# Kernel tuning notes

Hardware: AMD Instinct MI355X
Metric: run time of the kernel (lower is better)

The kernel has to match this reference:

```python
import jax, jax.numpy as jnp
import numpy as np

L = 2          # num_blocks
E = 256        # embed_features
FIN = 64       # input_features
FF = 4 * E     # dim_feedforward
OUT = 10       # out_dim
WCTX = 64      # context_len
B, S = 2, 1024
LN_EPS = 1e-5


def _ln(x, g, b):
    m = jnp.mean(x, axis=-1, keepdims=True)
    v = jnp.mean((x - m) ** 2, axis=-1, keepdims=True)
    return (x - m) / jnp.sqrt(v + LN_EPS) * g + b


def setup_inputs() -> dict:
    key = jax.random.key(0)
    ks = jax.random.split(key, 12)
    s = 0.02
    return {
        "inputs": jax.random.normal(ks[0], (B, S, FIN), jnp.float32),
        "embed_w": jax.random.normal(ks[1], (E, FIN), jnp.float32) * s,
        "embed_b": jnp.zeros((E,), jnp.float32),
        "qkv_w": jax.random.normal(ks[2], (L, 3 * E, E), jnp.float32) * s,
        "qkv_b": jnp.zeros((L, 3 * E), jnp.float32),
        "attn_out_w": jax.random.normal(ks[3], (L, E, E), jnp.float32) * s,
        "attn_out_b": jnp.zeros((L, E), jnp.float32),
        "ln1_g": jnp.ones((L, E), jnp.float32),
        "ln1_b": jnp.zeros((L, E), jnp.float32),
        "ffn1_w": jax.random.normal(ks[4], (L, FF, E), jnp.float32) * s,
        "ffn1_b": jnp.zeros((L, FF), jnp.float32),
        "ffn2_w": jax.random.normal(ks[5], (L, E, FF), jnp.float32) * s,
        "ffn2_b": jnp.zeros((L, E), jnp.float32),
        "ln2_g": jnp.ones((L, E), jnp.float32),
        "ln2_b": jnp.zeros((L, E), jnp.float32),
        "head_w": jax.random.normal(ks[6], (OUT, E), jnp.float32) * s,
        "head_b": jnp.zeros((OUT,), jnp.float32),
        "context_len": WCTX,
    }


def reference(inputs, embed_w, embed_b, qkv_w, qkv_b, attn_out_w, attn_out_b,
              ln1_g, ln1_b, ffn1_w, ffn1_b, ffn2_w, ffn2_b, ln2_g, ln2_b,
              head_w, head_b, context_len):
    b, s, _ = inputs.shape
    e = embed_w.shape[0]
    nh = max(1, e // 64) * 2           # torch: nhead = max(1, E//64)*2
    hd = e // nh
    scale = 1.0 / np.sqrt(hd)
    w = context_len

    emb = inputs @ embed_w.T + embed_b                       # [B,S,E]
    # left-pad with W-1 zeros so window pos p = padded[p:p+W] (zeros for early pos)
    padded = jnp.pad(emb, ((0, 0), (w - 1, 0), (0, 0)))
    idx = jnp.arange(s)[:, None] + jnp.arange(w)[None, :]    # [S,W]
    x = padded[:, idx].reshape(b * s, w, e)                  # [B*S,W,E]

    nlayers = qkv_w.shape[0]
    for l in range(nlayers):
        qkv = x @ qkv_w[l].T + qkv_b[l]                      # [N,W,3E]
        q, k, v = jnp.split(qkv, 3, axis=-1)
        q = q.reshape(-1, w, nh, hd)
        k = k.reshape(-1, w, nh, hd)
        v = v.reshape(-1, w, nh, hd)
        scores = jnp.einsum('nqhd,nkhd->nhqk', q, k) * scale
        attn = jax.nn.softmax(scores, axis=-1)
        o = jnp.einsum('nhqk,nkhd->nqhd', attn, v).reshape(-1, w, e)
        o = o @ attn_out_w[l].T + attn_out_b[l]
        x = _ln(x + o, ln1_g[l], ln1_b[l])                   # post-norm (torch default)
        ff = jax.nn.silu(x @ ffn1_w[l].T + ffn1_b[l]) @ ffn2_w[l].T + ffn2_b[l]
        x = _ln(x + ff, ln2_g[l], ln2_b[l])

    out = x[:, -1, :] @ head_w.T + head_b                    # last token of each window
    return out.reshape(b, s, -1)
```

## Files before the change

kernel.cpp:

```cpp
#include <hip/hip_runtime.h>
#include <hip/hip_bf16.h>

#define BB_ 2
#define SS_ 1024
#define FIN_ 64
#define EE_ 256
#define FF_ 1024
#define NH_ 8
#define HD_ 32
#define OUT_ 10
#define NWIN (BB_ * SS_)
#define NT 512
#define SCALE_ 0.17677669529663687f
#define XBP 264
#define TPAD 1088

typedef unsigned short u16;
typedef unsigned int u32;
typedef __attribute__((ext_vector_type(8))) short bf8_t;
typedef __attribute__((ext_vector_type(4))) float f4_t;
#define MFMA_B16(a, b, c) __builtin_amdgcn_mfma_f32_16x16x32_bf16(a, b, c, 0, 0, 0)

__device__ __forceinline__ u16 bf16r(float f) {
    u32 u = __builtin_bit_cast(u32, f);
    return (u16)((u + 0x7FFFu + ((u >> 16) & 1u)) >> 16);
}
__device__ __forceinline__ u32 pk_bf16(float a, float b) {
    return (u32)bf16r(a) | ((u32)bf16r(b) << 16);
}
__device__ __forceinline__ float b2f(u16 h) {
    return __builtin_bit_cast(float, ((u32)h) << 16);
}
__device__ __forceinline__ float b2f_lo(u32 u) {
    return __builtin_bit_cast(float, u << 16);
}
__device__ __forceinline__ float b2f_hi(u32 u) {
    return __builtin_bit_cast(float, u & 0xFFFF0000u);
}

__device__ __forceinline__ float dot4(float4 a, float4 b) {
    return a.x * b.x + a.y * b.y + a.z * b.z + a.w * b.w;
}
__device__ __forceinline__ float wsum(float v) {
#pragma unroll
    for (int o = 32; o > 0; o >>= 1) v += __shfl_xor(v, o, 64);
    return v;
}
__device__ __forceinline__ float wmax(float v) {
#pragma unroll
    for (int o = 32; o > 0; o >>= 1) v = fmaxf(v, __shfl_xor(v, o, 64));
    return v;
}
__device__ __forceinline__ float silu_f(float h) { return h / (1.f + __expf(-h)); }

struct CvtArgs {
    const float* s[9];
    u16* d[9];
    int n[9];
};

__global__ void k_pre(const float* __restrict__ in, const float* __restrict__ embw,
                      const float* __restrict__ embb, const float* __restrict__ qkv_b,
                      CvtArgs ca, float* __restrict__ emb, u16* __restrict__ qkvp) {
    __shared__ float row[FIN_];
    const int blk = blockIdx.x;
    const int tid = threadIdx.x;
    if (blk < 2048) {
        if (tid < FIN_) row[tid] = in[blk * FIN_ + tid];
        __syncthreads();
        const float4* w4 = (const float4*)(embw + tid * FIN_);
        const float4* r4 = (const float4*)row;
        float s = 0.f;
#pragma unroll
        for (int c = 0; c < FIN_ / 4; ++c) s += dot4(w4[c], r4[c]);
        emb[blk * EE_ + tid] = s + embb[tid];
    } else if (blk < 2816) {
        const int b2 = blk - 2048;
#pragma unroll 1
        for (int seg = 0; seg < 9; ++seg) {
            const float* __restrict__ src = ca.s[seg];
            u16* __restrict__ dst = ca.d[seg];
            const int nn = ca.n[seg];
            for (int i = b2 * 256 + tid; i < nn; i += 768 * 256)
                dst[i] = bf16r(src[i]);
        }
    } else {
        const int b3 = blk - 2816;
        for (int f = b3 * 256 + tid; f < 2 * 64 * 768; f += 8 * 256) {
            const int bat = f / 49152;
            const int rem = f - bat * 49152;
            const int r = rem / 768, cl = rem - r * 768;
            qkvp[((size_t)bat * TPAD + r) * 768 + cl] = bf16r(qkv_b[cl]);
        }
    }
}

__global__ __launch_bounds__(512) void k_qkv0m(const float* __restrict__ emb,
                                               const u16* __restrict__ wq0b,
                                               const float* __restrict__ qkvb,
                                               u16* __restrict__ qkvp) {
    __shared__ u16 ab[16 * XBP];
    const int b = blockIdx.x;
    const int tid = threadIdx.x, lane = tid & 63, wv = tid >> 6;
    const int col = lane & 15, quad = lane >> 4;
    for (int idx = tid; idx < 16 * 256; idx += 512) {
        const int i = idx >> 8, e = idx & 255;
        ab[i * XBP + e] = bf16r(emb[(b * 16 + i) * EE_ + e]);
    }
    __syncthreads();
    f4_t acc[6];
#pragma unroll
    for (int nt = 0; nt < 6; ++nt) acc[nt] = (f4_t){0.f, 0.f, 0.f, 0.f};
#pragma unroll
    for (int ks = 0; ks < 8; ++ks) {
        const bf8_t ax = *(const bf8_t*)(ab + col * XBP + ks * 32 + quad * 8);
#pragma unroll
        for (int nt = 0; nt < 6; ++nt) {
            const int r = wv * 96 + nt * 16 + col;
            const bf8_t bw = *(const bf8_t*)(wq0b + r * EE_ + ks * 32 + quad * 8);
            acc[nt] = MFMA_B16(ax, bw, acc[nt]);
        }
    }
#pragma unroll
    for (int nt = 0; nt < 6; ++nt) {
        const int cc = wv * 96 + nt * 16 + col;
        const float bs = qkvb[cc];
#pragma unroll
        for (int j = 0; j < 4; ++j) {
            const int tok = b * 16 + quad * 4 + j;
            const int bb = tok >> 10;
            const size_t ti = (size_t)bb * TPAD + (tok & 1023) + 64;
            qkvp[ti * 768 + cc] = bf16r(acc[nt][j] + bs);
        }
    }
}

__device__ __forceinline__ void reg_ln(float (&x)[2][4][4], float* red, float* stat,
                                       u16* xb,
                                       float gc0, float gc1, float bc0, float bc1,
                                       int tid, int wv, int col, int quad,
                                       int colg0, int colg1) {
    float ps[4][4], pq[4][4];
#pragma unroll
    for (int mt = 0; mt < 4; ++mt)
#pragma unroll
        for (int j = 0; j < 4; ++j) {
            const float v0 = x[0][mt][j], v1 = x[1][mt][j];
            ps[mt][j] = v0 + v1;
            pq[mt][j] = v0 * v0 + v1 * v1;
        }
#pragma unroll
    for (int o = 1; o < 16; o <<= 1) {
#pragma unroll
        for (int mt = 0; mt < 4; ++mt)
#pragma unroll
            for (int j = 0; j < 4; ++j) {
                ps[mt][j] += __shfl_xor(ps[mt][j], o);
                pq[mt][j] += __shfl_xor(pq[mt][j], o);
            }
    }
    if (col == 0) {
#pragma unroll
        for (int mt = 0; mt < 4; ++mt)
#pragma unroll
            for (int j = 0; j < 4; ++j) {
                const int row = mt * 16 + quad * 4 + j;
                red[row * 17 + wv * 2] = ps[mt][j];
                red[row * 17 + wv * 2 + 1] = pq[mt][j];
            }
    }
    __syncthreads();
    if (tid < 64) {
        float s = 0.f, q = 0.f;
#pragma unroll
        for (int w = 0; w < 8; ++w) {
            s += red[tid * 17 + w * 2];
            q += red[tid * 17 + w * 2 + 1];
        }
        const float m = s * 0.00390625f;
        const float var = q * 0.00390625f - m * m;
        stat[tid * 2] = m;
        stat[tid * 2 + 1] = rsqrtf(var + 1e-5f);
    }
    __syncthreads();
#pragma unroll
    for (int mt = 0; mt < 4; ++mt)
#pragma unroll
        for (int j = 0; j < 4; ++j) {
            const int row = mt * 16 + quad * 4 + j;
            const float m = stat[row * 2];
            const float rs = stat[row * 2 + 1];
            const float xn0 = (x[0][mt][j] - m) * rs * gc0 + bc0;
            const float xn1 = (x[1][mt][j] - m) * rs * gc1 + bc1;
            x[0][mt][j] = xn0;
            x[1][mt][j] = xn1;
            const u32 w = pk_bf16(xn0, xn1);
            xb[row * XBP + colg0] = (u16)w;
            xb[row * XBP + colg1] = (u16)(w >> 16);
        }
}

struct __align__(16) SMemA {
    union {
        struct { u16 qkpb[9216]; u16 vt[4608]; u16 pb[9216]; } att;
        struct { float red[64 * 17]; float stat[128]; } ln;
    } r1;
    u16 obxb[64 * XBP];
};

__global__ __launch_bounds__(NT, 4) void k_attn(
    const float* __restrict__ emb, const u16* __restrict__ qkvp,
    const u16* __restrict__ wob, const float* __restrict__ aob,
    const float* __restrict__ ln1g, const float* __restrict__ ln1b,
    u16* __restrict__ xbg) {
    __shared__ SMemA sm;
    const int n = blockIdx.x;
    const int bb = n >> 10, p = n & 1023;
    const int tid = threadIdx.x;
    const int lane = tid & 63, wv = tid >> 6;
    const int col = lane & 15, quad = lane >> 4;
    const int colg0 = wv * 32 + col, colg1 = colg0 + 16;

    for (int hp = 0; hp < 4; ++hp) {
        {
            const int i = tid >> 3, dg = tid & 7;
            const size_t rb = ((size_t)bb * TPAD + (p + 1 + i)) * 768 + hp * 64 + dg * 8;
            const uint4 q4 = *(const uint4*)(qkvp + rb);
            const uint4 k4 = *(const uint4*)(qkvp + rb + 256);
            const uint4 v4 = *(const uint4*)(qkvp + rb + 512);
            *(uint4*)(sm.r1.att.qkpb + i * 72 + dg * 8) = q4;
            *(uint4*)(sm.r1.att.qkpb + 4608 + i * 72 + dg * 8) = k4;
            union { uint4 u; u16 h[8]; } vu; vu.u = v4;
#pragma unroll
            for (int c = 0; c < 8; ++c)
                sm.r1.att.vt[(dg * 8 + c) * 72 + i] = vu.h[c];
        }
        __syncthreads();
        const int hh = wv >> 2, mt_ = wv & 3;
        const int r0 = mt_ * 16 + quad * 4;
        const bf8_t aq = *(const bf8_t*)(sm.r1.att.qkpb + (mt_ * 16 + col) * 72 + hh * 32 + quad * 8);
        f4_t sc[4];
#pragma unroll
        for (int nt = 0; nt < 4; ++nt) {
            const bf8_t bk = *(const bf8_t*)(sm.r1.att.qkpb + 4608 + (nt * 16 + col) * 72 + hh * 32 + quad * 8);
            f4_t z = {0.f, 0.f, 0.f, 0.f};
            sc[nt] = MFMA_B16(aq, bk, z);
        }
#pragma unroll
        for (int j = 0; j < 4; ++j) {
            float s0 = sc[0][j] * SCALE_, s1 = sc[1][j] * SCALE_;
            float s2v = sc[2][j] * SCALE_, s3 = sc[3][j] * SCALE_;
            float m = fmaxf(fmaxf(s0, s1), fmaxf(s2v, s3));
            m = fmaxf(m, __shfl_xor(m, 1)); m = fmaxf(m, __shfl_xor(m, 2));
            m = fmaxf(m, __shfl_xor(m, 4)); m = fmaxf(m, __shfl_xor(m, 8));
            const float e0 = __expf(s0 - m), e1 = __expf(s1 - m);
            const float e2 = __expf(s2v - m), e3 = __expf(s3 - m);
            float s = e0 + e1 + e2 + e3;
            s += __shfl_xor(s, 1); s += __shfl_xor(s, 2);
            s += __shfl_xor(s, 4); s += __shfl_xor(s, 8);
            const float inv = 1.f / s;
            sc[0][j] = e0 * inv; sc[1][j] = e1 * inv;
            sc[2][j] = e2 * inv; sc[3][j] = e3 * inv;
        }
        u16* pbh = sm.r1.att.pb + hh * 4608;
#pragma unroll
        for (int nt = 0; nt < 4; ++nt) {
            const u32 w01 = pk_bf16(sc[nt][0], sc[nt][1]);
            const u32 w23 = pk_bf16(sc[nt][2], sc[nt][3]);
            u16* pp = pbh + r0 * 72 + nt * 16 + col;
            pp[0] = (u16)w01; pp[72] = (u16)(w01 >> 16);
            pp[144] = (u16)w23; pp[216] = (u16)(w23 >> 16);
        }
        f4_t ov[2];
        ov[0] = (f4_t){0.f, 0.f, 0.f, 0.f}; ov[1] = (f4_t){0.f, 0.f, 0.f, 0.f};
#pragma unroll
        for (int ks = 0; ks < 2; ++ks) {
            const bf8_t ap = *(const bf8_t*)(pbh + (mt_ * 16 + col) * 72 + ks * 32 + quad * 8);
#pragma unroll
            for (int ntl = 0; ntl < 2; ++ntl) {
                const bf8_t bv = *(const bf8_t*)(sm.r1.att.vt +
                                                 (hh * 32 + ntl * 16 + col) * 72 + ks * 32 + quad * 8);
                ov[ntl] = MFMA_B16(ap, bv, ov[ntl]);
            }
        }
#pragma unroll
        for (int ntl = 0; ntl < 2; ++ntl) {
            const u32 w01 = pk_bf16(ov[ntl][0], ov[ntl][1]);
            const u32 w23 = pk_bf16(ov[ntl][2], ov[ntl][3]);
            u16* oo = sm.obxb + r0 * XBP + (hp * 2 + hh) * 32 + ntl * 16 + col;
            oo[0] = (u16)w01; oo[XBP] = (u16)(w01 >> 16);
            oo[2 * XBP] = (u16)w23; oo[3 * XBP] = (u16)(w23 >> 16);
        }
        __syncthreads();
    }

    f4_t pacc[2][4];
#pragma unroll
    for (int a = 0; a < 2; ++a)
#pragma unroll
        for (int m = 0; m < 4; ++m) pacc[a][m] = (f4_t){0.f, 0.f, 0.f, 0.f};
#pragma unroll 2
    for (int ks = 0; ks < 8; ++ks) {
        bf8_t ao[4];
#pragma unroll
        for (int mt = 0; mt < 4; ++mt)
            ao[mt] = *(const bf8_t*)(sm.obxb + (mt * 16 + col) * XBP + ks * 32 + quad * 8);
#pragma unroll
        for (int ntl = 0; ntl < 2; ++ntl) {
            const bf8_t bw = *(const bf8_t*)(wob + ((wv * 2 + ntl) * 16 + col) * EE_ +
                                             ks * 32 + quad * 8);
#pragma unroll
            for (int mt = 0; mt < 4; ++mt) pacc[ntl][mt] = MFMA_B16(ao[mt], bw, pacc[ntl][mt]);
        }
    }

    const float aob_0 = aob[colg0], aob_1 = aob[colg1];
    float x[2][4][4];
#pragma unroll
    for (int mt = 0; mt < 4; ++mt)
#pragma unroll
        for (int j = 0; j < 4; ++j) {
            const int row = mt * 16 + quad * 4 + j;
            const int t = p - 63 + row;
            const size_t base = (size_t)((bb << 10) + t) * EE_;
            const float e0 = (t >= 0) ? emb[base + colg0] : 0.f;
            const float e1 = (t >= 0) ? emb[base + colg1] : 0.f;
            x[0][mt][j] = e0 + aob_0 + pacc[0][mt][j];
            x[1][mt][j] = e1 + aob_1 + pacc[1][mt][j];
        }
    __syncthreads();
    reg_ln(x, sm.r1.ln.red, sm.r1.ln.stat, sm.obxb,
           ln1g[colg0], ln1g[colg1], ln1b[colg0], ln1b[colg1],
           tid, wv, col, quad, colg0, colg1);
    __syncthreads();
    u16* dst = xbg + (size_t)n * 64 * 256;
#pragma unroll
    for (int k = 0; k < 4; ++k) {
        const int idx = tid + k * NT;
        const int row = idx >> 5, seg = idx & 31;
        *(uint4*)(dst + row * 256 + seg * 8) = *(const uint4*)(sm.obxb + row * XBP + seg * 8);
    }
}

struct __align__(16) SMemB {
    u16 xb[64 * XBP];
    union {
        u16 hb2[2][64 * 136];
        u16 kvb[4 * 64 * 66];
        struct { float red[64 * 17]; float stat[128]; } ln;
    } c;
    float x1row[256];
    float o1b[256];
    float q1b[256];
    float sbuf2[256];
};

__global__ __launch_bounds__(NT, 4) void k_mlp(
    const u16* __restrict__ xbg,
    const u16* __restrict__ w1b, const u16* __restrict__ w2b,
    const u16* __restrict__ wkvb, const u16* __restrict__ wq1b,
    const u16* __restrict__ wob1,
    const float* __restrict__ qkv_b, const float* __restrict__ aob,
    const float* __restrict__ f1b, const float* __restrict__ f2b,
    const float* __restrict__ ln2g, const float* __restrict__ ln2b,
    float* __restrict__ x2g) {
    __shared__ SMemB sm;
    const int n = blockIdx.x;
    const int tid = threadIdx.x;
    const int lane = tid & 63, wv = tid >> 6;
    const int col = lane & 15, quad = lane >> 4;
    const int colg0 = wv * 32 + col, colg1 = colg0 + 16;

    const float* qkv_b1 = qkv_b + 3 * EE_;
    const float* aob1p = aob + EE_;

    const u16* src = xbg + (size_t)n * 64 * 256;
#pragma unroll
    for (int k = 0; k < 4; ++k) {
        const int idx = tid + k * NT;
        const int row = idx >> 5, seg = idx & 31;
        *(uint4*)(sm.xb + row * XBP + seg * 8) = *(const uint4*)(src + row * 256 + seg * 8);
    }
    __syncthreads();

    f4_t facc[2][4];
#pragma unroll
    for (int a = 0; a < 2; ++a)
#pragma unroll
        for (int m = 0; m < 4; ++m) facc[a][m] = (f4_t){0.f, 0.f, 0.f, 0.f};

    auto ffn1_step = [&](int c) {
        f4_t hacc[4];
#pragma unroll
        for (int m = 0; m < 4; ++m) hacc[m] = (f4_t){0.f, 0.f, 0.f, 0.f};
        const int f = c * 128 + wv * 16 + col;
#pragma unroll 2
        for (int ks = 0; ks < 8; ++ks) {
            const bf8_t bw = *(const bf8_t*)(w1b + f * EE_ + ks * 32 + quad * 8);
#pragma unroll
            for (int mt = 0; mt < 4; ++mt) {
                const bf8_t axr = *(const bf8_t*)(sm.xb + (mt * 16 + col) * XBP + ks * 32 + quad * 8);
                hacc[mt] = MFMA_B16(axr, bw, hacc[mt]);
            }
        }
        const float bv = f1b[f];
        const int lc = wv * 16 + col;
        u16* hbc = sm.c.hb2[c & 1];
#pragma unroll
        for (int mt = 0; mt < 4; ++mt) {
            const u32 w01 = pk_bf16(silu_f(hacc[mt][0] + bv), silu_f(hacc[mt][1] + bv));
            const u32 w23 = pk_bf16(silu_f(hacc[mt][2] + bv), silu_f(hacc[mt][3] + bv));
            u16* hh2 = hbc + (mt * 16 + quad * 4) * 136 + lc;
            hh2[0] = (u16)w01; hh2[136] = (u16)(w01 >> 16);
            hh2[272] = (u16)w23; hh2[408] = (u16)(w23 >> 16);
        }
    };
    auto ffn2_step = [&](int c) {
        const u16* hbc = sm.c.hb2[c & 1];
#pragma unroll 2
        for (int ks = 0; ks < 4; ++ks) {
            bf8_t ah[4];
#pragma unroll
            for (int mt = 0; mt < 4; ++mt)
                ah[mt] = *(const bf8_t*)(hbc + (mt * 16 + col) * 136 + ks * 32 + quad * 8);
#pragma unroll
            for (int ntl = 0; ntl < 2; ++ntl) {
                const int e = (wv * 2 + ntl) * 16 + col;
                const bf8_t bw = *(const bf8_t*)(w2b + e * FF_ + c * 128 + ks * 32 + quad * 8);
#pragma unroll
                for (int mt = 0; mt < 4; ++mt) facc[ntl][mt] = MFMA_B16(ah[mt], bw, facc[ntl][mt]);
            }
        }
    };

    ffn1_step(0);
    __syncthreads();
#pragma unroll 1
    for (int c = 0; c < 8; ++c) {
        if (c < 7) ffn1_step(c + 1);
        ffn2_step(c);
        __syncthreads();
    }

    const float f2b_0 = f2b[colg0], f2b_1 = f2b[colg1];
    float x[2][4][4];
#pragma unroll
    for (int mt = 0; mt < 4; ++mt)
#pragma unroll
        for (int j = 0; j < 4; ++j) {
            const int row = mt * 16 + quad * 4 + j;
            x[0][mt][j] = b2f(sm.xb[row * XBP + colg0]) + facc[0][mt][j] + f2b_0;
            x[1][mt][j] = b2f(sm.xb[row * XBP + colg1]) + facc[1][mt][j] + f2b_1;
        }
    __syncthreads();
    reg_ln(x, sm.c.ln.red, sm.c.ln.stat, sm.xb,
           ln2g[colg0], ln2g[colg1], ln2b[colg0], ln2b[colg1],
           tid, wv, col, quad, colg0, colg1);
    if (quad == 3) {
        sm.x1row[colg0] = x[0][3][3];
        sm.x1row[colg1] = x[1][3][3];
    }
    __syncthreads();

#pragma unroll 1
    for (int chunk = 0; chunk < 2; ++chunk) {
        {
            const int hpc = wv & 1, hf = (wv >> 1) & 1, mtkh = (wv >> 2) & 1;
            const int hpg = chunk * 2 + hpc;
            f4_t kacc[2][4];
#pragma unroll
            for (int a = 0; a < 2; ++a)
#pragma unroll
                for (int b = 0; b < 4; ++b) kacc[a][b] = (f4_t){0.f, 0.f, 0.f, 0.f};
#pragma unroll 2
            for (int ks = 0; ks < 8; ++ks) {
                bf8_t ax[2];
#pragma unroll
                for (int m2 = 0; m2 < 2; ++m2)
                    ax[m2] = *(const bf8_t*)(sm.xb + ((mtkh * 2 + m2) * 16 + col) * XBP + ks * 32 + quad * 8);
#pragma unroll
                for (int nt = 0; nt < 4; ++nt) {
                    const int wr = hf * EE_ + hpg * 64 + nt * 16 + col;
                    const bf8_t bw = *(const bf8_t*)(wkvb + wr * EE_ + ks * 32 + quad * 8);
#pragma unroll
                    for (int m2 = 0; m2 < 2; ++m2) kacc[m2][nt] = MFMA_B16(ax[m2], bw, kacc[m2][nt]);
                }
            }
            u16* dst = sm.c.kvb + (hpc * 2 + hf) * 4224;
#pragma unroll
            for (int m2 = 0; m2 < 2; ++m2)
#pragma unroll
                for (int nt = 0; nt < 4; ++nt) {
                    const int cc = nt * 16 + col;
                    const float bs = qkv_b1[(hf + 1) * EE_ + hpg * 64 + cc];
                    const u32 w01 = pk_bf16(kacc[m2][nt][0] + bs, kacc[m2][nt][1] + bs);
                    const u32 w23 = pk_bf16(kacc[m2][nt][2] + bs, kacc[m2][nt][3] + bs);
                    u16* dd = dst + ((mtkh * 2 + m2) * 16 + quad * 4) * 66 + cc;
                    dd[0] = (u16)w01; dd[66] = (u16)(w01 >> 16);
                    dd[132] = (u16)w23; dd[198] = (u16)(w23 >> 16);
                }
        }
        if (chunk == 0 && tid < 256) {
            const u16* wq = wq1b + tid * EE_;
            float s = 0.f;
#pragma unroll 8
            for (int k2 = 0; k2 < 128; ++k2) {
                const u32 u = *(const u32*)(wq + k2 * 2);
                s += sm.x1row[2 * k2] * b2f_lo(u) + sm.x1row[2 * k2 + 1] * b2f_hi(u);
            }
            sm.q1b[tid] = s + qkv_b1[tid];
        }
        __syncthreads();
        if (tid < 256) {
            const int hc = tid >> 6, jj = tid & 63;
            const int hpc = hc >> 1, hh = hc & 1;
            const u16* kr = sm.c.kvb + (hpc * 2) * 4224 + jj * 66 + hh * 32;
            const float* qv = sm.q1b + (chunk * 4 + hc) * 32;
            float s = 0.f;
#pragma unroll
            for (int d = 0; d < 32; ++d) s += qv[d] * b2f(kr[d]);
            s *= SCALE_;
            const float m = wmax(s);
            const float e = __expf(s - m);
            const float su = wsum(e);
            sm.sbuf2[hc * 64 + jj] = e / su;
        }
        __syncthreads();
        if (tid < 128) {
            const int hc = tid >> 5, d = tid & 31;
            const int hpc = hc >> 1, hh = hc & 1;
            const u16* vr = sm.c.kvb + (hpc * 2 + 1) * 4224 + hh * 32 + d;
            float acc = 0.f;
            for (int j = 0; j < 64; ++j)
                acc += sm.sbuf2[hc * 64 + j] * b2f(vr[j * 66]);
            sm.o1b[(chunk * 4 + hc) * 32 + d] = acc;
        }
        __syncthreads();
    }

    if (tid < 256) {
        const u16* wr = wob1 + tid * EE_;
        float s = 0.f;
#pragma unroll 8
        for (int k2 = 0; k2 < 128; ++k2) {
            const u32 u = *(const u32*)(wr + k2 * 2);
            s += sm.o1b[2 * k2] * b2f_lo(u) + sm.o1b[2 * k2 + 1] * b2f_hi(u);
        }
        x2g[n * EE_ + tid] = sm.x1row[tid] + s + aob1p[tid];
    }
}

__global__ __launch_bounds__(256) void k_tail(
    const float* __restrict__ x2g, const u16* __restrict__ w1b1,
    const float* __restrict__ f1b1, const u16* __restrict__ w2b1,
    const float* __restrict__ f2b1, const float* __restrict__ g1,
    const float* __restrict__ b1, const float* __restrict__ g2,
    const float* __restrict__ b2, const float* __restrict__ hw,
    const float* __restrict__ hbb, float* __restrict__ out) {
    __shared__ float xa[4 * 260];
    __shared__ float hid[4 * 1024];
    const int tid = threadIdx.x, lane = tid & 63, w = tid >> 6;
    const int n0 = blockIdx.x * 4;
    {
        const float* src = x2g + (size_t)(n0 + w) * EE_;
        const float v0 = src[lane], v1 = src[lane + 64], v2 = src[lane + 128], v3 = src[lane + 192];
        const float m = wsum(v0 + v1 + v2 + v3) * 0.00390625f;
        const float d0 = v0 - m, d1 = v1 - m, d2 = v2 - m, d3 = v3 - m;
        const float var = wsum(d0 * d0 + d1 * d1 + d2 * d2 + d3 * d3) * 0.00390625f;
        const float rs = rsqrtf(var + 1e-5f);
        xa[w * 260 + lane] = d0 * rs * g1[lane] + b1[lane];
        xa[w * 260 + lane + 64] = d1 * rs * g1[lane + 64] + b1[lane + 64];
        xa[w * 260 + lane + 128] = d2 * rs * g1[lane + 128] + b1[lane + 128];
        xa[w * 260 + lane + 192] = d3 * rs * g1[lane + 192] + b1[lane + 192];
    }
    __syncthreads();
#pragma unroll 1
    for (int r = 0; r < 4; ++r) {
        const int f = r * 256 + tid;
        const u16* wrow = w1b1 + f * EE_;
        float a0 = 0.f, a1 = 0.f, a2 = 0.f, a3 = 0.f;
#pragma unroll 4
        for (int k2 = 0; k2 < 128; ++k2) {
            const u32 u = *(const u32*)(wrow + k2 * 2);
            const float lo = b2f_lo(u), hi = b2f_hi(u);
            const float2 h0 = *(const float2*)(xa + 0 * 260 + k2 * 2);
            const float2 h1 = *(const float2*)(xa + 1 * 260 + k2 * 2);
            const float2 h2 = *(const float2*)(xa + 2 * 260 + k2 * 2);
            const float2 h3 = *(const float2*)(xa + 3 * 260 + k2 * 2);
            a0 += h0.x * lo + h0.y * hi;
            a1 += h1.x * lo + h1.y * hi;
            a2 += h2.x * lo + h2.y * hi;
            a3 += h3.x * lo + h3.y * hi;
        }
        const float bv = f1b1[f];
        hid[0 * 1024 + f] = silu_f(a0 + bv);
        hid[1 * 1024 + f] = silu_f(a1 + bv);
        hid[2 * 1024 + f] = silu_f(a2 + bv);
        hid[3 * 1024 + f] = silu_f(a3 + bv);
    }
    __syncthreads();
    {
        const u16* wrow = w2b1 + tid * FF_;
        float a0 = 0.f, a1 = 0.f, a2 = 0.f, a3 = 0.f;
#pragma unroll 4
        for (int k2 = 0; k2 < 512; ++k2) {
            const u32 u = *(const u32*)(wrow + k2 * 2);
            const float lo = b2f_lo(u), hi = b2f_hi(u);
            const float2 h0 = *(const float2*)(hid + 0 * 1024 + k2 * 2);
            const float2 h1 = *(const float2*)(hid + 1 * 1024 + k2 * 2);
            const float2 h2 = *(const float2*)(hid + 2 * 1024 + k2 * 2);
            const float2 h3 = *(const float2*)(hid + 3 * 1024 + k2 * 2);
            a0 += h0.x * lo + h0.y * hi;
            a1 += h1.x * lo + h1.y * hi;
            a2 += h2.x * lo + h2.y * hi;
            a3 += h3.x * lo + h3.y * hi;
        }
        const float bv = f2b1[tid];
        const float r0 = xa[0 * 260 + tid] + a0 + bv;
        const float r1 = xa[1 * 260 + tid] + a1 + bv;
        const float r2 = xa[2 * 260 + tid] + a2 + bv;
        const float r3 = xa[3 * 260 + tid] + a3 + bv;
        __syncthreads();
        xa[0 * 260 + tid] = r0;
        xa[1 * 260 + tid] = r1;
        xa[2 * 260 + tid] = r2;
        xa[3 * 260 + tid] = r3;
    }
    __syncthreads();
    {
        float* row = xa + w * 260;
        const float v0 = row[lane], v1 = row[lane + 64], v2 = row[lane + 128], v3 = row[lane + 192];
        const float m = wsum(v0 + v1 + v2 + v3) * 0.00390625f;
        const float d0 = v0 - m, d1 = v1 - m, d2 = v2 - m, d3 = v3 - m;
        const float var = wsum(d0 * d0 + d1 * d1 + d2 * d2 + d3 * d3) * 0.00390625f;
        const float rs = rsqrtf(var + 1e-5f);
        __syncthreads();
        row[lane] = d0 * rs * g2[lane] + b2[lane];
        row[lane + 64] = d1 * rs * g2[lane + 64] + b2[lane + 64];
        row[lane + 128] = d2 * rs * g2[lane + 128] + b2[lane + 128];
        row[lane + 192] = d3 * rs * g2[lane + 192] + b2[lane + 192];
    }
    __syncthreads();
    if (tid < 4 * OUT_) {
        const int win = tid / OUT_, o = tid % OUT_;
        const float* wr = hw + o * EE_;
        const float* xr = xa + win * 260;
        float s = 0.f;
#pragma unroll 8
        for (int c4 = 0; c4 < 64; ++c4)
            s += dot4(*(const float4*)(xr + c4 * 4), *(const float4*)(wr + c4 * 4));
        out[(n0 + win) * OUT_ + o] = s + hbb[o];
    }
}

extern "C" void kernel_launch(void* const* d_in, const int* in_sizes, int n_in,
                              void* d_out, int out_size, void* d_ws, size_t ws_size,
                              hipStream_t stream) {
    (void)in_sizes; (void)n_in; (void)out_size; (void)ws_size;
    const float* inputs = (const float*)d_in[0];
    const float* embed_w = (const float*)d_in[1];
    const float* embed_b = (const float*)d_in[2];
    const float* qkv_w = (const float*)d_in[3];
    const float* qkv_b = (const float*)d_in[4];
    const float* attn_out_w = (const float*)d_in[5];
    const float* attn_out_b = (const float*)d_in[6];
    const float* ln1_g = (const float*)d_in[7];
    const float* ln1_b = (const float*)d_in[8];
    const float* ffn1_w = (const float*)d_in[9];
    const float* ffn1_b = (const float*)d_in[10];
    const float* ffn2_w = (const float*)d_in[11];
    const float* ffn2_b = (const float*)d_in[12];
    const float* ln2_g = (const float*)d_in[13];
    const float* ln2_b = (const float*)d_in[14];
    const float* head_w = (const float*)d_in[15];
    const float* head_b = (const float*)d_in[16];
    float* out = (float*)d_out;

    char* wsb = (char*)d_ws;
    size_t off = 0;
    auto alloc = [&](size_t bytes) { char* pp = wsb + off; off += (bytes + 511) & ~511ull; return pp; };
    float* emb   = (float*)alloc((size_t)NWIN * EE_ * 4);
    u16*   qkvp  = (u16*)alloc((size_t)BB_ * TPAD * 768 * 2);
    u16*   xbg   = (u16*)alloc((size_t)NWIN * 64 * 256 * 2);
    float* x2g   = (float*)alloc((size_t)NWIN * EE_ * 4);
    u16*   w1b   = (u16*)alloc(FF_ * EE_ * 2);
    u16*   w2b   = (u16*)alloc(EE_ * FF_ * 2);
    u16*   wob   = (u16*)alloc(EE_ * EE_ * 2);
    u16*   wkvb  = (u16*)alloc(2 * EE_ * EE_ * 2);
    u16*   w1b1  = (u16*)alloc(FF_ * EE_ * 2);
    u16*   w2b1  = (u16*)alloc(EE_ * FF_ * 2);
    u16*   wob1  = (u16*)alloc(EE_ * EE_ * 2);
    u16*   wq1b  = (u16*)alloc(EE_ * EE_ * 2);
    u16*   wq0b  = (u16*)alloc(3 * EE_ * EE_ * 2);

    CvtArgs ca;
    ca.s[0] = ffn1_w;                            ca.d[0] = w1b;  ca.n[0] = FF_ * EE_;
    ca.s[1] = ffn2_w;                            ca.d[1] = w2b;  ca.n[1] = EE_ * FF_;
    ca.s[2] = attn_out_w;                        ca.d[2] = wob;  ca.n[2] = EE_ * EE_;
    ca.s[3] = qkv_w + 3 * EE_ * EE_ + EE_ * EE_; ca.d[3] = wkvb; ca.n[3] = 2 * EE_ * EE_;
    ca.s[4] = ffn1_w + FF_ * EE_;                ca.d[4] = w1b1; ca.n[4] = FF_ * EE_;
    ca.s[5] = ffn2_w + EE_ * FF_;                ca.d[5] = w2b1; ca.n[5] = EE_ * FF_;
    ca.s[6] = attn_out_w + EE_ * EE_;            ca.d[6] = wob1; ca.n[6] = EE_ * EE_;
    ca.s[7] = qkv_w + 3 * EE_ * EE_;             ca.d[7] = wq1b; ca.n[7] = EE_ * EE_;
    ca.s[8] = qkv_w;                             ca.d[8] = wq0b; ca.n[8] = 3 * EE_ * EE_;

    k_pre<<<2824, 256, 0, stream>>>(inputs, embed_w, embed_b, qkv_b, ca, emb, qkvp);
    k_qkv0m<<<NWIN / 16, 512, 0, stream>>>(emb, wq0b, qkv_b, qkvp);
    k_attn<<<NWIN, NT, 0, stream>>>(emb, qkvp, wob, attn_out_b, ln1_g, ln1_b, xbg);
    k_mlp<<<NWIN, NT, 0, stream>>>(xbg, w1b, w2b, wkvb, wq1b, wob1,
                                   qkv_b, attn_out_b, ffn1_b, ffn2_b,
                                   ln2_g, ln2_b, x2g);
    k_tail<<<NWIN / 4, 256, 0, stream>>>(x2g, w1b1, ffn1_b + FF_, w2b1, ffn2_b + EE_,
                                         ln1_g + EE_, ln1_b + EE_, ln2_g + EE_, ln2_b + EE_,
                                         head_w, head_b, out);
}
```

Before: 795.6 us.

## Split fused MLP+layer1 attention kernel into separate FFN and layer-1 kernels

```diff
diff --git a/kernel.cpp b/kernel.cpp
--- a/kernel.cpp
+++ b/kernel.cpp
@@ -342,44 +342,32 @@
     }
 }
 
-struct __align__(16) SMemB {
+struct __align__(16) SMemF {
     u16 xb[64 * XBP];
     union {
         u16 hb2[2][64 * 136];
-        u16 kvb[4 * 64 * 66];
         struct { float red[64 * 17]; float stat[128]; } ln;
     } c;
-    float x1row[256];
-    float o1b[256];
-    float q1b[256];
-    float sbuf2[256];
 };
 
-__global__ __launch_bounds__(NT, 4) void k_mlp(
-    const u16* __restrict__ xbg,
+__global__ __launch_bounds__(NT, 4) void k_ffn(
+    u16* __restrict__ xbg,
     const u16* __restrict__ w1b, const u16* __restrict__ w2b,
-    const u16* __restrict__ wkvb, const u16* __restrict__ wq1b,
-    const u16* __restrict__ wob1,
-    const float* __restrict__ qkv_b, const float* __restrict__ aob,
     const float* __restrict__ f1b, const float* __restrict__ f2b,
-    const float* __restrict__ ln2g, const float* __restrict__ ln2b,
-    float* __restrict__ x2g) {
-    __shared__ SMemB sm;
+    const float* __restrict__ ln2g, const float* __restrict__ ln2b) {
+    __shared__ SMemF sm;
     const int n = blockIdx.x;
     const int tid = threadIdx.x;
     const int lane = tid & 63, wv = tid >> 6;
     const int col = lane & 15, quad = lane >> 4;
     const int colg0 = wv * 32 + col, colg1 = colg0 + 16;
 
-    const float* qkv_b1 = qkv_b + 3 * EE_;
-    const float* aob1p = aob + EE_;
-
-    const u16* src = xbg + (size_t)n * 64 * 256;
+    u16* gptr = xbg + (size_t)n * 64 * 256;
 #pragma unroll
     for (int k = 0; k < 4; ++k) {
         const int idx = tid + k * NT;
         const int row = idx >> 5, seg = idx & 31;
-        *(uint4*)(sm.xb + row * XBP + seg * 8) = *(const uint4*)(src + row * 256 + seg * 8);
+        *(uint4*)(sm.xb + row * XBP + seg * 8) = *(const uint4*)(gptr + row * 256 + seg * 8);
     }
     __syncthreads();
 
@@ -456,10 +444,47 @@
     reg_ln(x, sm.c.ln.red, sm.c.ln.stat, sm.xb,
            ln2g[colg0], ln2g[colg1], ln2b[colg0], ln2b[colg1],
            tid, wv, col, quad, colg0, colg1);
-    if (quad == 3) {
-        sm.x1row[colg0] = x[0][3][3];
-        sm.x1row[colg1] = x[1][3][3];
-    }
+    __syncthreads();
+#pragma unroll
+    for (int k = 0; k < 4; ++k) {
+        const int idx = tid + k * NT;
+        const int row = idx >> 5, seg = idx & 31;
+        *(uint4*)(gptr + row * 256 + seg * 8) = *(const uint4*)(sm.xb + row * XBP + seg * 8);
+    }
+}
+
+struct __align__(16) SMemL {
+    u16 xb[64 * XBP];
+    u16 kvb[4 * 64 * 66];
+    float x1row[256];
+    float o1b[256];
+    float q1b[256];
+    float sbuf2[256];
+};
+
+__global__ __launch_bounds__(NT, 4) void k_l1(
+    const u16* __restrict__ xbg,
+    const u16* __restrict__ wkvb, const u16* __restrict__ wq1b,
+    const u16* __restrict__ wob1,
+    const float* __restrict__ qkv_b, const float* __restrict__ aob,
+    float* __restrict__ x2g) {
+    __shared__ SMemL sm;
+    const int n = blockIdx.x;
+    const int tid = threadIdx.x;
+    const int lane = tid & 63, wv = tid >> 6;
+    const int col = lane & 15, quad = lane >> 4;
+
+    const float* qkv_b1 = qkv_b + 3 * EE_;
+    const float* aob1p = aob + EE_;
+
+    const u16* src = xbg + (size_t)n * 64 * 256;
+#pragma unroll
+    for (int k = 0; k < 4; ++k) {
+        const int idx = tid + k * NT;
+        const int row = idx >> 5, seg = idx & 31;
+        *(uint4*)(sm.xb + row * XBP + seg * 8) = *(const uint4*)(src + row * 256 + seg * 8);
+    }
+    if (tid < 256) sm.x1row[tid] = b2f(src[63 * 256 + tid]);
     __syncthreads();
 
 #pragma unroll 1
@@ -486,7 +511,7 @@
                     for (int m2 = 0; m2 < 2; ++m2) kacc[m2][nt] = MFMA_B16(ax[m2], bw, kacc[m2][nt]);
                 }
             }
-            u16* dst = sm.c.kvb + (hpc * 2 + hf) * 4224;
+            u16* dst = sm.kvb + (hpc * 2 + hf) * 4224;
 #pragma unroll
             for (int m2 = 0; m2 < 2; ++m2)
 #pragma unroll
@@ -514,7 +539,7 @@
         if (tid < 256) {
             const int hc = tid >> 6, jj = tid & 63;
             const int hpc = hc >> 1, hh = hc & 1;
-            const u16* kr = sm.c.kvb + (hpc * 2) * 4224 + jj * 66 + hh * 32;
+            const u16* kr = sm.kvb + (hpc * 2) * 4224 + jj * 66 + hh * 32;
             const float* qv = sm.q1b + (chunk * 4 + hc) * 32;
             float s = 0.f;
 #pragma unroll
@@ -529,7 +554,7 @@
         if (tid < 128) {
             const int hc = tid >> 5, d = tid & 31;
             const int hpc = hc >> 1, hh = hc & 1;
-            const u16* vr = sm.c.kvb + (hpc * 2 + 1) * 4224 + hh * 32 + d;
+            const u16* vr = sm.kvb + (hpc * 2 + 1) * 4224 + hh * 32 + d;
             float acc = 0.f;
             for (int j = 0; j < 64; ++j)
                 acc += sm.sbuf2[hc * 64 + j] * b2f(vr[j * 66]);
@@ -707,9 +732,8 @@
     k_pre<<<2824, 256, 0, stream>>>(inputs, embed_w, embed_b, qkv_b, ca, emb, qkvp);
     k_qkv0m<<<NWIN / 16, 512, 0, stream>>>(emb, wq0b, qkv_b, qkvp);
     k_attn<<<NWIN, NT, 0, stream>>>(emb, qkvp, wob, attn_out_b, ln1_g, ln1_b, xbg);
-    k_mlp<<<NWIN, NT, 0, stream>>>(xbg, w1b, w2b, wkvb, wq1b, wob1,
-                                   qkv_b, attn_out_b, ffn1_b, ffn2_b,
-                                   ln2_g, ln2_b, x2g);
+    k_ffn<<<NWIN, NT, 0, stream>>>(xbg, w1b, w2b, ffn1_b, ffn2_b, ln2_g, ln2_b);
+    k_l1<<<NWIN, NT, 0, stream>>>(xbg, wkvb, wq1b, wob1, qkv_b, attn_out_b, x2g);
     k_tail<<<NWIN / 4, 256, 0, stream>>>(x2g, w1b1, ffn1_b + FF_, w2b1, ffn2_b + EE_,
                                          ln1_g + EE_, ln1_b + EE_, ln2_g + EE_, ln2_b + EE_,
                                          head_w, head_b, out);
```

Result: slower. 831.4 us (+4.5%).
